# Performance work log

Measured on AMD Instinct MI355X. Metric: run time of the kernel, lower is better.

## Reference

```python
import jax, jax.numpy as jnp
import numpy as np

N = 100000   # nodes
E1 = 300000  # GINEConv (down) edges
E2 = 150000  # GraphConv (up) edges
D = 256      # hidden_dim
BN_EPS = 1e-5


def _bn_eval(h, gamma, beta, mean, var):
    # BatchNorm1d in eval mode (running stats)
    return (h - mean) * (gamma / jnp.sqrt(var + BN_EPS)) + beta


def setup_inputs() -> dict:
    key = jax.random.key(0)
    ks = jax.random.split(key, 12)
    s = 1.0 / np.sqrt(D)
    inp = {
        # forward args
        "x": jax.random.normal(ks[0], (N, D), dtype=jnp.float32),
        "edge_index": jax.random.randint(ks[1], (2, E1), 0, N, dtype=jnp.int64),
        "edge_attr_emb": jax.random.normal(ks[2], (E1, D), dtype=jnp.float32),
        "v_idx": jax.random.randint(ks[3], (2, E2), 0, N, dtype=jnp.int64),
        # GINEConv params
        "eps": jnp.zeros((), dtype=jnp.float32),  # train_eps, init 0
        "w1a": jax.random.normal(ks[4], (D, D), dtype=jnp.float32) * s,
        "b1a": jnp.zeros((D,), dtype=jnp.float32),
        "bn1_g": jnp.ones((D,), dtype=jnp.float32),
        "bn1_b": jnp.zeros((D,), dtype=jnp.float32),
        "bn1_m": jnp.zeros((D,), dtype=jnp.float32),
        "bn1_v": jnp.ones((D,), dtype=jnp.float32),
        "w1b": jax.random.normal(ks[5], (D, D), dtype=jnp.float32) * s,
        "b1b": jnp.zeros((D,), dtype=jnp.float32),
        # GraphConv params (lin_rel has bias, lin_root has no bias)
        "gc_w_rel": jax.random.normal(ks[6], (D, D), dtype=jnp.float32) * s,
        "gc_b_rel": jnp.zeros((D,), dtype=jnp.float32),
        "gc_w_root": jax.random.normal(ks[7], (D, D), dtype=jnp.float32) * s,
        # residual mixing + outer BN
        "alpha1": jnp.float32(0.5),
        "alpha2": jnp.float32(0.5),
        "bn_g": jnp.ones((D,), dtype=jnp.float32),
        "bn_b": jnp.zeros((D,), dtype=jnp.float32),
        "bn_m": jnp.zeros((D,), dtype=jnp.float32),
        "bn_v": jnp.ones((D,), dtype=jnp.float32),
    }
    return inp


def reference(x, edge_index, edge_attr_emb, v_idx, eps,
              w1a, b1a, bn1_g, bn1_b, bn1_m, bn1_v, w1b, b1b,
              gc_w_rel, gc_b_rel, gc_w_root,
              alpha1, alpha2, bn_g, bn_b, bn_m, bn_v):
    # ----- GINEConv: out = nn((1+eps)*x + sum_j relu(x_j + e_ji)) -----
    src, dst = edge_index[0], edge_index[1]
    msg = jax.nn.relu(x[src] + edge_attr_emb)                 # [E1, D] gather + add
    aggr = jax.ops.segment_sum(msg, dst, num_segments=N)      # scatter-add -> [N, D]
    h = (1.0 + eps) * x + aggr
    # nn1: Linear -> BN(eval) -> ReLU -> Dropout(eval=id) -> Linear
    h = jax.nn.relu(_bn_eval(h @ w1a.T + b1a, bn1_g, bn1_b, bn1_m, bn1_v))
    h_down = h @ w1b.T + b1b

    # ----- GraphConv (aggr='add'): lin_rel(sum_j x_j) + lin_root(x) -----
    src2, dst2 = v_idx[0], v_idx[1]
    aggr2 = jax.ops.segment_sum(x[src2], dst2, num_segments=N)  # [N, D]
    h_up = aggr2 @ gc_w_rel.T + gc_b_rel + x @ gc_w_root.T

    # ----- residual mix + BN + ReLU -----
    out = x + alpha1 * h_down + alpha2 * h_up
    return jax.nn.relu(_bn_eval(out, bn_g, bn_b, bn_m, bn_v))
```

## Files before the change

### kernel.cpp

```cpp
#include <hip/hip_runtime.h>
#include <hip/hip_bf16.h>

typedef __bf16 bf16_t;
typedef bf16_t bf16x8 __attribute__((ext_vector_type(8)));
typedef bf16_t bf16x4 __attribute__((ext_vector_type(4)));
typedef float  f32x4  __attribute__((ext_vector_type(4)));

#define NN 100000
#define E1N 300000
#define E2N 150000
#define DD 256
#define BNEPS 1e-5f

#define SWZ(row, col) ((col) ^ (((row) & 7) << 3))

__device__ __forceinline__ void glds16(const bf16_t* src, bf16_t* ldsbase) {
  __builtin_amdgcn_global_load_lds(
      (const __attribute__((address_space(1))) void*)src,
      (__attribute__((address_space(3))) void*)ldsbase, 16, 0, 0);
}

__global__ void prep_scalars(const float* b1a, const float* g1, const float* be1,
                             const float* m1, const float* v1,
                             const float* b1b, const float* gbrel,
                             const float* a1p, const float* a2p,
                             const float* g2, const float* be2,
                             const float* m2, const float* v2,
                             float* fold1, float* c2, float* s2f) {
  int c = threadIdx.x;
  float s1 = g1[c] * rsqrtf(v1[c] + BNEPS);
  fold1[c] = (b1a[c] - m1[c]) * s1 + be1[c];
  float s2 = g2[c] * rsqrtf(v2[c] + BNEPS);
  float cst = a1p[0] * b1b[c] + a2p[0] * gbrel[c];
  c2[c] = (cst - m2[c]) * s2 + be2[c];
  s2f[c] = s2;
}

__global__ void prep_w1(const float* w1a, const float* g1, const float* v1,
                        bf16_t* w1ab) {
  int o = blockIdx.x, i = threadIdx.x;
  float s1 = g1[o] * rsqrtf(v1[o] + BNEPS);
  w1ab[o * DD + i] = (bf16_t)(w1a[o * DD + i] * s1);
}

__global__ void prep_w2(const float* w1b, const float* wrel, const float* wroot,
                        const float* a1p, const float* a2p,
                        const float* g2, const float* v2, bf16_t* w2f) {
  int o = blockIdx.x, i = threadIdx.x;
  float s2 = g2[o] * rsqrtf(v2[o] + BNEPS);
  float a1 = a1p[0], a2 = a2p[0];
  w2f[o * 768 + i]       = (bf16_t)(w1b[o * DD + i]   * a1 * s2);
  w2f[o * 768 + 256 + i] = (bf16_t)(wrel[o * DD + i]  * a2 * s2);
  w2f[o * 768 + 512 + i] = (bf16_t)(wroot[o * DD + i] * a2 * s2);
}

__global__ void cast_x(const float* __restrict__ x, bf16_t* __restrict__ xbf) {
  size_t i = (size_t)(blockIdx.x * 256 + threadIdx.x) * 8;
  f32x4 v0 = *(const f32x4*)(x + i);
  f32x4 v1 = *(const f32x4*)(x + i + 4);
  bf16x8 o;
#pragma unroll
  for (int j = 0; j < 4; ++j) { o[j] = (bf16_t)v0[j]; o[4 + j] = (bf16_t)v1[j]; }
  *(bf16x8*)(xbf + i) = o;
}

__global__ void init_heads(int* head1, int* head2) {
  int i = blockIdx.x * 256 + threadIdx.x;
  if (i < NN) { head1[i] = -1; head2[i] = -1; }
}

__global__ void build_lists(const int* __restrict__ ei, const int* __restrict__ vi,
                            int* head1, int* next1, int* head2, int* next2) {
  int e = blockIdx.x * 256 + threadIdx.x;
  if (e < E1N) {
    int dst = ei[E1N + e];
    next1[e] = atomicExch(head1 + dst, e);
  }
  if (e < E2N) {
    int dst = vi[E2N + e];
    next2[e] = atomicExch(head2 + dst, e);
  }
}

__global__ __launch_bounds__(256) void aggregate(
    const bf16_t* __restrict__ xbf, const float* epsp,
    const int* __restrict__ ei, const float* __restrict__ eattr,
    const int* __restrict__ vi,
    const int* __restrict__ head1, const int* __restrict__ next1,
    const int* __restrict__ head2, const int* __restrict__ next2,
    bf16_t* __restrict__ aggr1_bf, bf16_t* __restrict__ aggr2_bf) {
  int n = blockIdx.x * 4 + (threadIdx.x >> 6);
  int lane = threadIdx.x & 63;
  int col = lane * 4;
  float sc = 1.0f + epsp[0];
  bf16x4 xv = *(const bf16x4*)(xbf + (size_t)n * DD + col);
  f32x4 acc1, acc2 = {0.f, 0.f, 0.f, 0.f};
#pragma unroll
  for (int j = 0; j < 4; ++j) acc1[j] = (float)xv[j] * sc;

  for (int e = head1[n]; e >= 0; e = next1[e]) {
    int src = ei[e];
    bf16x4 a = *(const bf16x4*)(xbf + (size_t)src * DD + col);
    f32x4 b = *(const f32x4*)(eattr + (size_t)e * DD + col);
#pragma unroll
    for (int j = 0; j < 4; ++j) {
      float m = (float)a[j] + b[j];
      acc1[j] += (m > 0.f ? m : 0.f);
    }
  }
  for (int e = head2[n]; e >= 0; e = next2[e]) {
    int src = vi[e];
    bf16x4 a = *(const bf16x4*)(xbf + (size_t)src * DD + col);
#pragma unroll
    for (int j = 0; j < 4; ++j) acc2[j] += (float)a[j];
  }

  bf16x4 o1, o2;
#pragma unroll
  for (int j = 0; j < 4; ++j) { o1[j] = (bf16_t)acc1[j]; o2[j] = (bf16_t)acc2[j]; }
  *(bf16x4*)(aggr1_bf + (size_t)n * DD + col) = o1;
  *(bf16x4*)(aggr2_bf + (size_t)n * DD + col) = o2;
}

__global__ __launch_bounds__(512) void gemm1(const bf16_t* __restrict__ aggr1_bf,
                                             const bf16_t* __restrict__ w1ab,
                                             const float* __restrict__ fold1,
                                             bf16_t* __restrict__ t1) {
  __shared__ bf16_t As[128][64];
  __shared__ bf16_t Bs[256][64];
  const int tid = threadIdx.x;
  const int m0 = blockIdx.x * 128;
  const int lane = tid & 63, wid = tid >> 6;
  const int wr = wid >> 2, wc = wid & 3;
  const int lr = lane & 15, kg = (lane >> 4) * 8;
  const int lrow = lane >> 3;
  const int lcol = ((lane & 7) ^ (lane >> 3)) * 8;

  f32x4 acc[4][4] = {};

  for (int kt = 0; kt < 4; ++kt) {
    const int k0 = kt * 64;
#pragma unroll
    for (int i = 0; i < 2; ++i) {
      int r0 = wid * 16 + i * 8;
      glds16(aggr1_bf + (size_t)(m0 + r0 + lrow) * DD + k0 + lcol, &As[r0][0]);
    }
#pragma unroll
    for (int i = 0; i < 4; ++i) {
      int r0 = wid * 32 + i * 8;
      glds16(w1ab + (size_t)(r0 + lrow) * DD + k0 + lcol, &Bs[r0][0]);
    }
    __syncthreads();
#pragma unroll
    for (int kk = 0; kk < 2; ++kk) {
      bf16x8 af[4], bfr[4];
#pragma unroll
      for (int m = 0; m < 4; ++m) {
        int r = wr * 64 + m * 16 + lr;
        af[m] = *(const bf16x8*)&As[r][SWZ(r, kk * 32 + kg)];
      }
#pragma unroll
      for (int n = 0; n < 4; ++n) {
        int r = wc * 64 + n * 16 + lr;
        bfr[n] = *(const bf16x8*)&Bs[r][SWZ(r, kk * 32 + kg)];
      }
#pragma unroll
      for (int m = 0; m < 4; ++m)
#pragma unroll
        for (int n = 0; n < 4; ++n)
          acc[m][n] = __builtin_amdgcn_mfma_f32_16x16x32_bf16(af[m], bfr[n], acc[m][n], 0, 0, 0);
    }
    __syncthreads();
  }

  const int rg = lane >> 4;
#pragma unroll
  for (int n = 0; n < 4; ++n) {
    int gc = wc * 64 + n * 16 + lr;
    float fo = fold1[gc];
#pragma unroll
    for (int m = 0; m < 4; ++m) {
      int gr0 = m0 + wr * 64 + m * 16 + rg * 4;
#pragma unroll
      for (int r = 0; r < 4; ++r) {
        int gr = gr0 + r;
        if (gr < NN) {
          float v = acc[m][n][r] + fo;
          t1[(size_t)gr * DD + gc] = (bf16_t)(v > 0.f ? v : 0.f);
        }
      }
    }
  }
}

__global__ __launch_bounds__(512) void gemm2(const bf16_t* __restrict__ t1,
                                             const bf16_t* __restrict__ aggr2_bf,
                                             const bf16_t* __restrict__ xbf,
                                             const bf16_t* __restrict__ w2f,
                                             const float* __restrict__ c2,
                                             const float* __restrict__ s2f,
                                             float* __restrict__ out) {
  __shared__ bf16_t As[128][64];
  __shared__ bf16_t Bs[256][64];
  const int tid = threadIdx.x;
  const int m0 = blockIdx.x * 128;
  const int lane = tid & 63, wid = tid >> 6;
  const int wr = wid >> 2, wc = wid & 3;
  const int lr = lane & 15, kg = (lane >> 4) * 8;
  const int lrow = lane >> 3;
  const int lcol = ((lane & 7) ^ (lane >> 3)) * 8;

  f32x4 acc[4][4] = {};

  for (int kt = 0; kt < 12; ++kt) {
    const bf16_t* Asrc = (kt < 4) ? t1 : (kt < 8 ? aggr2_bf : xbf);
    const int k0 = (kt & 3) * 64;
#pragma unroll
    for (int i = 0; i < 2; ++i) {
      int r0 = wid * 16 + i * 8;
      glds16(Asrc + (size_t)(m0 + r0 + lrow) * DD + k0 + lcol, &As[r0][0]);
    }
#pragma unroll
    for (int i = 0; i < 4; ++i) {
      int r0 = wid * 32 + i * 8;
      glds16(w2f + (size_t)(r0 + lrow) * 768 + kt * 64 + lcol, &Bs[r0][0]);
    }
    __syncthreads();
#pragma unroll
    for (int kk = 0; kk < 2; ++kk) {
      bf16x8 af[4], bfr[4];
#pragma unroll
      for (int m = 0; m < 4; ++m) {
        int r = wr * 64 + m * 16 + lr;
        af[m] = *(const bf16x8*)&As[r][SWZ(r, kk * 32 + kg)];
      }
#pragma unroll
      for (int n = 0; n < 4; ++n) {
        int r = wc * 64 + n * 16 + lr;
        bfr[n] = *(const bf16x8*)&Bs[r][SWZ(r, kk * 32 + kg)];
      }
#pragma unroll
      for (int m = 0; m < 4; ++m)
#pragma unroll
        for (int n = 0; n < 4; ++n)
          acc[m][n] = __builtin_amdgcn_mfma_f32_16x16x32_bf16(af[m], bfr[n], acc[m][n], 0, 0, 0);
    }
    __syncthreads();
  }

  const int rg = lane >> 4;
#pragma unroll
  for (int n = 0; n < 4; ++n) {
    int gc = wc * 64 + n * 16 + lr;
    float c2v = c2[gc];
    float s2v = s2f[gc];
#pragma unroll
    for (int m = 0; m < 4; ++m) {
      int gr0 = m0 + wr * 64 + m * 16 + rg * 4;
#pragma unroll
      for (int r = 0; r < 4; ++r) {
        int gr = gr0 + r;
        if (gr < NN) {
          float v = acc[m][n][r] + c2v + (float)xbf[(size_t)gr * DD + gc] * s2v;
          out[(size_t)gr * DD + gc] = (v > 0.f ? v : 0.f);
        }
      }
    }
  }
}

extern "C" void kernel_launch(void* const* d_in, const int* in_sizes, int n_in,
                              void* d_out, int out_size, void* d_ws, size_t ws_size,
                              hipStream_t stream) {
  const float* x     = (const float*)d_in[0];
  const int*   ei    = (const int*)d_in[1];
  const float* eattr = (const float*)d_in[2];
  const int*   vi    = (const int*)d_in[3];
  const float* epsp  = (const float*)d_in[4];
  const float* w1a   = (const float*)d_in[5];
  const float* b1a   = (const float*)d_in[6];
  const float* bn1g  = (const float*)d_in[7];
  const float* bn1b  = (const float*)d_in[8];
  const float* bn1m  = (const float*)d_in[9];
  const float* bn1v  = (const float*)d_in[10];
  const float* w1b   = (const float*)d_in[11];
  const float* b1b   = (const float*)d_in[12];
  const float* wrel  = (const float*)d_in[13];
  const float* gbrel = (const float*)d_in[14];
  const float* wroot = (const float*)d_in[15];
  const float* a1p   = (const float*)d_in[16];
  const float* a2p   = (const float*)d_in[17];
  const float* bng   = (const float*)d_in[18];
  const float* bnb   = (const float*)d_in[19];
  const float* bnm   = (const float*)d_in[20];
  const float* bnv   = (const float*)d_in[21];

  char* ws = (char*)d_ws;
  bf16_t* aggr1_bf = (bf16_t*)ws;
  bf16_t* aggr2_bf = (bf16_t*)(ws + 51200000);
  bf16_t* xbf      = (bf16_t*)(ws + 102400000);
  bf16_t* t1       = (bf16_t*)(ws + 153600000);
  bf16_t* w1ab     = (bf16_t*)(ws + 204800000);
  bf16_t* w2f      = (bf16_t*)(ws + 204931072);
  float*  fold1    = (float*)(ws + 205324288);
  float*  c2       = (float*)(ws + 205325312);
  float*  s2f      = (float*)(ws + 205326336);
  int*    head1    = (int*)(ws + 205327360);
  int*    head2    = (int*)(ws + 205727360);
  int*    next1    = (int*)(ws + 206127360);
  int*    next2    = (int*)(ws + 207327360);

  prep_scalars<<<1, 256, 0, stream>>>(b1a, bn1g, bn1b, bn1m, bn1v, b1b, gbrel,
                                      a1p, a2p, bng, bnb, bnm, bnv, fold1, c2, s2f);
  prep_w1<<<256, 256, 0, stream>>>(w1a, bn1g, bn1v, w1ab);
  prep_w2<<<256, 256, 0, stream>>>(w1b, wrel, wroot, a1p, a2p, bng, bnv, w2f);
  cast_x<<<12500, 256, 0, stream>>>(x, xbf);
  init_heads<<<391, 256, 0, stream>>>(head1, head2);
  build_lists<<<1172, 256, 0, stream>>>(ei, vi, head1, next1, head2, next2);
  aggregate<<<25000, 256, 0, stream>>>(xbf, epsp, ei, eattr, vi,
                                       head1, next1, head2, next2,
                                       aggr1_bf, aggr2_bf);
  gemm1<<<782, 512, 0, stream>>>(aggr1_bf, w1ab, fold1, t1);
  gemm2<<<782, 512, 0, stream>>>(t1, aggr2_bf, xbf, w2f, c2, s2f, (float*)d_out);
}
```

Before: 344.8 us.

## Fuse both GEMMs via LDS-resident intermediate and split aggregation across wavefronts

The two GEMM kernels become one. The first GEMM's ReLU output tile (128x256 bf16) stays in swizzled shared memory and is read directly as the first K-slices of the second GEMM, so t1 is never written to or read back from global memory. The aggregation kernel now gives the GINE and GraphConv neighbor walks to separate wavefronts per node, which doubles the block count and shortens each wave's serial dependency chain. Head initialization is also folded into the cast kernel to save a launch. The extra 64 KB of LDS per block raises shared-memory use and may lower occupancy of the fused GEMM.

Result: slower. 357.9 us (+3.8%).

```diff
diff --git a/kernel.cpp b/kernel.cpp
--- a/kernel.cpp
+++ b/kernel.cpp
@@ -13,6 +13,7 @@
 #define BNEPS 1e-5f
 
 #define SWZ(row, col) ((col) ^ (((row) & 7) << 3))
+#define SWZ256(row, col) (((col) & 192) | (((col) & 63) ^ (((row) & 7) << 3)))
 
 __device__ __forceinline__ void glds16(const bf16_t* src, bf16_t* ldsbase) {
   __builtin_amdgcn_global_load_lds(
@@ -54,19 +55,17 @@
   w2f[o * 768 + 512 + i] = (bf16_t)(wroot[o * DD + i] * a2 * s2);
 }
 
-__global__ void cast_x(const float* __restrict__ x, bf16_t* __restrict__ xbf) {
-  size_t i = (size_t)(blockIdx.x * 256 + threadIdx.x) * 8;
+__global__ void cast_x(const float* __restrict__ x, bf16_t* __restrict__ xbf,
+                       int* __restrict__ head1, int* __restrict__ head2) {
+  int gid = blockIdx.x * 256 + threadIdx.x;
+  size_t i = (size_t)gid * 8;
   f32x4 v0 = *(const f32x4*)(x + i);
   f32x4 v1 = *(const f32x4*)(x + i + 4);
   bf16x8 o;
 #pragma unroll
   for (int j = 0; j < 4; ++j) { o[j] = (bf16_t)v0[j]; o[4 + j] = (bf16_t)v1[j]; }
   *(bf16x8*)(xbf + i) = o;
-}
-
-__global__ void init_heads(int* head1, int* head2) {
-  int i = blockIdx.x * 256 + threadIdx.x;
-  if (i < NN) { head1[i] = -1; head2[i] = -1; }
+  if (gid < NN) { head1[gid] = -1; head2[gid] = -1; }
 }
 
 __global__ void build_lists(const int* __restrict__ ei, const int* __restrict__ vi,
@@ -89,45 +88,56 @@
     const int* __restrict__ head1, const int* __restrict__ next1,
     const int* __restrict__ head2, const int* __restrict__ next2,
     bf16_t* __restrict__ aggr1_bf, bf16_t* __restrict__ aggr2_bf) {
-  int n = blockIdx.x * 4 + (threadIdx.x >> 6);
+  int n = blockIdx.x * 2 + (threadIdx.x >> 7);
+  int role = (threadIdx.x >> 6) & 1;
   int lane = threadIdx.x & 63;
   int col = lane * 4;
-  float sc = 1.0f + epsp[0];
-  bf16x4 xv = *(const bf16x4*)(xbf + (size_t)n * DD + col);
-  f32x4 acc1, acc2 = {0.f, 0.f, 0.f, 0.f};
-#pragma unroll
-  for (int j = 0; j < 4; ++j) acc1[j] = (float)xv[j] * sc;
-
-  for (int e = head1[n]; e >= 0; e = next1[e]) {
-    int src = ei[e];
-    bf16x4 a = *(const bf16x4*)(xbf + (size_t)src * DD + col);
-    f32x4 b = *(const f32x4*)(eattr + (size_t)e * DD + col);
-#pragma unroll
-    for (int j = 0; j < 4; ++j) {
-      float m = (float)a[j] + b[j];
-      acc1[j] += (m > 0.f ? m : 0.f);
-    }
-  }
-  for (int e = head2[n]; e >= 0; e = next2[e]) {
-    int src = vi[e];
-    bf16x4 a = *(const bf16x4*)(xbf + (size_t)src * DD + col);
-#pragma unroll
-    for (int j = 0; j < 4; ++j) acc2[j] += (float)a[j];
-  }
-
-  bf16x4 o1, o2;
-#pragma unroll
-  for (int j = 0; j < 4; ++j) { o1[j] = (bf16_t)acc1[j]; o2[j] = (bf16_t)acc2[j]; }
-  *(bf16x4*)(aggr1_bf + (size_t)n * DD + col) = o1;
-  *(bf16x4*)(aggr2_bf + (size_t)n * DD + col) = o2;
-}
-
-__global__ __launch_bounds__(512) void gemm1(const bf16_t* __restrict__ aggr1_bf,
-                                             const bf16_t* __restrict__ w1ab,
-                                             const float* __restrict__ fold1,
-                                             bf16_t* __restrict__ t1) {
+
+  if (role == 0) {
+    float sc = 1.0f + epsp[0];
+    bf16x4 xv = *(const bf16x4*)(xbf + (size_t)n * DD + col);
+    f32x4 acc1;
+#pragma unroll
+    for (int j = 0; j < 4; ++j) acc1[j] = (float)xv[j] * sc;
+    for (int e = head1[n]; e >= 0; e = next1[e]) {
+      int src = ei[e];
+      bf16x4 a = *(const bf16x4*)(xbf + (size_t)src * DD + col);
+      f32x4 b = *(const f32x4*)(eattr + (size_t)e * DD + col);
+#pragma unroll
+      for (int j = 0; j < 4; ++j) {
+        float m = (float)a[j] + b[j];
+        acc1[j] += (m > 0.f ? m : 0.f);
+      }
+    }
+    bf16x4 o1;
+#pragma unroll
+    for (int j = 0; j < 4; ++j) o1[j] = (bf16_t)acc1[j];
+    *(bf16x4*)(aggr1_bf + (size_t)n * DD + col) = o1;
+  } else {
+    f32x4 acc2 = {0.f, 0.f, 0.f, 0.f};
+    for (int e = head2[n]; e >= 0; e = next2[e]) {
+      int src = vi[e];
+      bf16x4 a = *(const bf16x4*)(xbf + (size_t)src * DD + col);
+#pragma unroll
+      for (int j = 0; j < 4; ++j) acc2[j] += (float)a[j];
+    }
+    bf16x4 o2;
+#pragma unroll
+    for (int j = 0; j < 4; ++j) o2[j] = (bf16_t)acc2[j];
+    *(bf16x4*)(aggr2_bf + (size_t)n * DD + col) = o2;
+  }
+}
+
+__global__ __launch_bounds__(512) void gemm_fused(
+    const bf16_t* __restrict__ aggr1_bf, const bf16_t* __restrict__ w1ab,
+    const float* __restrict__ fold1,
+    const bf16_t* __restrict__ aggr2_bf, const bf16_t* __restrict__ xbf,
+    const bf16_t* __restrict__ w2f,
+    const float* __restrict__ c2, const float* __restrict__ s2f,
+    float* __restrict__ out) {
   __shared__ bf16_t As[128][64];
   __shared__ bf16_t Bs[256][64];
+  __shared__ bf16_t T1[128][256];
   const int tid = threadIdx.x;
   const int m0 = blockIdx.x * 128;
   const int lane = tid & 63, wid = tid >> 6;
@@ -135,6 +145,7 @@
   const int lr = lane & 15, kg = (lane >> 4) * 8;
   const int lrow = lane >> 3;
   const int lcol = ((lane & 7) ^ (lane >> 3)) * 8;
+  const int rg = lane >> 4;
 
   f32x4 acc[4][4] = {};
 
@@ -173,52 +184,33 @@
     __syncthreads();
   }
 
-  const int rg = lane >> 4;
 #pragma unroll
   for (int n = 0; n < 4; ++n) {
     int gc = wc * 64 + n * 16 + lr;
     float fo = fold1[gc];
 #pragma unroll
     for (int m = 0; m < 4; ++m) {
-      int gr0 = m0 + wr * 64 + m * 16 + rg * 4;
+      int r0 = wr * 64 + m * 16 + rg * 4;
 #pragma unroll
       for (int r = 0; r < 4; ++r) {
-        int gr = gr0 + r;
-        if (gr < NN) {
-          float v = acc[m][n][r] + fo;
-          t1[(size_t)gr * DD + gc] = (bf16_t)(v > 0.f ? v : 0.f);
-        }
-      }
-    }
-  }
-}
-
-__global__ __launch_bounds__(512) void gemm2(const bf16_t* __restrict__ t1,
-                                             const bf16_t* __restrict__ aggr2_bf,
-                                             const bf16_t* __restrict__ xbf,
-                                             const bf16_t* __restrict__ w2f,
-                                             const float* __restrict__ c2,
-                                             const float* __restrict__ s2f,
-                                             float* __restrict__ out) {
-  __shared__ bf16_t As[128][64];
-  __shared__ bf16_t Bs[256][64];
-  const int tid = threadIdx.x;
-  const int m0 = blockIdx.x * 128;
-  const int lane = tid & 63, wid = tid >> 6;
-  const int wr = wid >> 2, wc = wid & 3;
-  const int lr = lane & 15, kg = (lane >> 4) * 8;
-  const int lrow = lane >> 3;
-  const int lcol = ((lane & 7) ^ (lane >> 3)) * 8;
-
-  f32x4 acc[4][4] = {};
+        int row = r0 + r;
+        float v = acc[m][n][r] + fo;
+        T1[row][SWZ256(row, gc)] = (bf16_t)(v > 0.f ? v : 0.f);
+        acc[m][n][r] = 0.f;
+      }
+    }
+  }
+  __syncthreads();
 
   for (int kt = 0; kt < 12; ++kt) {
-    const bf16_t* Asrc = (kt < 4) ? t1 : (kt < 8 ? aggr2_bf : xbf);
     const int k0 = (kt & 3) * 64;
-#pragma unroll
-    for (int i = 0; i < 2; ++i) {
-      int r0 = wid * 16 + i * 8;
-      glds16(Asrc + (size_t)(m0 + r0 + lrow) * DD + k0 + lcol, &As[r0][0]);
+    if (kt >= 4) {
+      const bf16_t* Asrc = (kt < 8) ? aggr2_bf : xbf;
+#pragma unroll
+      for (int i = 0; i < 2; ++i) {
+        int r0 = wid * 16 + i * 8;
+        glds16(Asrc + (size_t)(m0 + r0 + lrow) * DD + k0 + lcol, &As[r0][0]);
+      }
     }
 #pragma unroll
     for (int i = 0; i < 4; ++i) {
@@ -232,7 +224,9 @@
 #pragma unroll
       for (int m = 0; m < 4; ++m) {
         int r = wr * 64 + m * 16 + lr;
-        af[m] = *(const bf16x8*)&As[r][SWZ(r, kk * 32 + kg)];
+        af[m] = (kt < 4)
+          ? *(const bf16x8*)&T1[r][SWZ256(r, k0 + kk * 32 + kg)]
+          : *(const bf16x8*)&As[r][SWZ(r, kk * 32 + kg)];
       }
 #pragma unroll
       for (int n = 0; n < 4; ++n) {
@@ -248,7 +242,6 @@
     __syncthreads();
   }
 
-  const int rg = lane >> 4;
 #pragma unroll
   for (int n = 0; n < 4; ++n) {
     int gc = wc * 64 + n * 16 + lr;
@@ -299,27 +292,26 @@
   bf16_t* aggr1_bf = (bf16_t*)ws;
   bf16_t* aggr2_bf = (bf16_t*)(ws + 51200000);
   bf16_t* xbf      = (bf16_t*)(ws + 102400000);
-  bf16_t* t1       = (bf16_t*)(ws + 153600000);
-  bf16_t* w1ab     = (bf16_t*)(ws + 204800000);
-  bf16_t* w2f      = (bf16_t*)(ws + 204931072);
-  float*  fold1    = (float*)(ws + 205324288);
-  float*  c2       = (float*)(ws + 205325312);
-  float*  s2f      = (float*)(ws + 205326336);
-  int*    head1    = (int*)(ws + 205327360);
-  int*    head2    = (int*)(ws + 205727360);
-  int*    next1    = (int*)(ws + 206127360);
-  int*    next2    = (int*)(ws + 207327360);
+  bf16_t* w1ab     = (bf16_t*)(ws + 153600000);
+  bf16_t* w2f      = (bf16_t*)(ws + 153731072);
+  float*  fold1    = (float*)(ws + 154124288);
+  float*  c2       = (float*)(ws + 154125312);
+  float*  s2f      = (float*)(ws + 154126336);
+  int*    head1    = (int*)(ws + 154127360);
+  int*    head2    = (int*)(ws + 154527360);
+  int*    next1    = (int*)(ws + 154927360);
+  int*    next2    = (int*)(ws + 156127360);
 
   prep_scalars<<<1, 256, 0, stream>>>(b1a, bn1g, bn1b, bn1m, bn1v, b1b, gbrel,
                                       a1p, a2p, bng, bnb, bnm, bnv, fold1, c2, s2f);
   prep_w1<<<256, 256, 0, stream>>>(w1a, bn1g, bn1v, w1ab);
   prep_w2<<<256, 256, 0, stream>>>(w1b, wrel, wroot, a1p, a2p, bng, bnv, w2f);
-  cast_x<<<12500, 256, 0, stream>>>(x, xbf);
-  init_heads<<<391, 256, 0, stream>>>(head1, head2);
+  cast_x<<<12500, 256, 0, stream>>>(x, xbf, head1, head2);
   build_lists<<<1172, 256, 0, stream>>>(ei, vi, head1, next1, head2, next2);
-  aggregate<<<25000, 256, 0, stream>>>(xbf, epsp, ei, eattr, vi,
+  aggregate<<<50000, 256, 0, stream>>>(xbf, epsp, ei, eattr, vi,
                                        head1, next1, head2, next2,
                                        aggr1_bf, aggr2_bf);
-  gemm1<<<782, 512, 0, stream>>>(aggr1_bf, w1ab, fold1, t1);
-  gemm2<<<782, 512, 0, stream>>>(t1, aggr2_bf, xbf, w2f, c2, s2f, (float*)d_out);
-}
+  gemm_fused<<<782, 512, 0, stream>>>(aggr1_bf, w1ab, fold1,
+                                      aggr2_bf, xbf, w2f, c2, s2f,
+                                      (float*)d_out);
+}
```
